# Performance work log

Hardware: AMD Instinct MI355X
Metric: run time of the kernel (lower is better)

## Reference

```python
import jax, jax.numpy as jnp
import numpy as np

N_NODES = 50000

def _gcn_layer(x, src, dst, W, b, n_nodes):
    # x: [N, F_in]; src/dst: [E+N] (self-loops already appended)
    h = x @ W  # [N, F_out]
    deg = jax.ops.segment_sum(jnp.ones_like(dst, dtype=h.dtype), dst, num_segments=n_nodes)
    dinv = jnp.where(deg > 0, jax.lax.rsqrt(deg), 0.0)  # deg^{-1/2}
    norm = dinv[src] * dinv[dst]  # [E+N]
    msg = h[src] * norm[:, None]  # gather + scale
    out = jax.ops.segment_sum(msg, dst, num_segments=n_nodes)  # scatter-add
    return out + b

def setup_inputs() -> dict:
    key = jax.random.key(0)
    k1, k2, k3, k4 = jax.random.split(key, 4)
    d = 128
    E = 800000
    x = jax.random.normal(k1, (N_NODES, d), dtype=jnp.float32)
    edge_index = jax.random.randint(k2, (2, E), 0, N_NODES, dtype=jnp.int64)
    W1 = jax.random.normal(k3, (d, d), dtype=jnp.float32) / np.sqrt(d)
    b1 = jnp.zeros((d,), dtype=jnp.float32)
    W2 = jax.random.normal(k4, (d, d), dtype=jnp.float32) / np.sqrt(d)
    b2 = jnp.zeros((d,), dtype=jnp.float32)
    return {"x": x, "edge_index": edge_index, "W1": W1, "b1": b1, "W2": W2, "b2": b2}

def reference(x, edge_index, W1, b1, W2, b2):
    n = x.shape[0]
    loops = jnp.arange(n, dtype=edge_index.dtype)
    src = jnp.concatenate([edge_index[0], loops])  # add self-loops
    dst = jnp.concatenate([edge_index[1], loops])
    h = _gcn_layer(x, src, dst, W1, b1, n)
    h = jax.nn.relu(h)
    z = _gcn_layer(h, src, dst, W2, b2, n)
    return z
```

## Files before the change

### kernel.cpp

```cpp
#include <hip/hip_runtime.h>
#include <hip/hip_fp16.h>

#define NF 128
#define DMAX 64

typedef _Float16 half8  __attribute__((ext_vector_type(8)));
typedef _Float16 half4v __attribute__((ext_vector_type(4)));
typedef float    floatx4 __attribute__((ext_vector_type(4)));

__global__ __launch_bounds__(256) void z_k(
    int* __restrict__ cnt, int N, int zb,
    const float* __restrict__ W1, const float* __restrict__ W2,
    __half* __restrict__ WT1, __half* __restrict__ WT2)
{
    int b = blockIdx.x;
    if (b < zb) {
        int i = b * 256 + threadIdx.x;
        if (i <= N) cnt[i] = 0;
        return;
    }
    int idx = (b - zb) * 256 + threadIdx.x;
    const float* W = (idx < 16384) ? W1 : W2;
    __half* WT     = (idx < 16384) ? WT1 : WT2;
    int j = idx & 16383;
    int nn = j & 127, k = j >> 7;
    WT[nn * NF + k] = __float2half(W[k * NF + nn]);
}

__device__ __forceinline__ void gemm1raw_body(
    const float* __restrict__ X, const __half* __restrict__ WT,
    float* __restrict__ H32, int M, int bid, __half (*wlds)[136])
{
    const int tid = threadIdx.x;
    {
        int r = tid >> 2;
        int c0 = (tid & 3) * 32;
        const half8* s = (const half8*)(WT + (size_t)r * NF + c0);
        half8* d = (half8*)&wlds[r][c0];
        #pragma unroll
        for (int j = 0; j < 4; j++) d[j] = s[j];
    }
    __syncthreads();

    const int wave = tid >> 6, lane = tid & 63;
    const int quad = lane >> 4, l15 = lane & 15;
    const int rowA = bid * 128 + wave * 16 + l15;
    const int rowc = (rowA < M) ? rowA : (M - 1);

    half8 afr[4];
    #pragma unroll
    for (int kc = 0; kc < 4; kc++) {
        const floatx4* p = (const floatx4*)(X + (size_t)rowc * NF + kc * 32 + quad * 8);
        floatx4 u = p[0], v = p[1];
        half8 a;
        a[0] = (_Float16)u[0]; a[1] = (_Float16)u[1];
        a[2] = (_Float16)u[2]; a[3] = (_Float16)u[3];
        a[4] = (_Float16)v[0]; a[5] = (_Float16)v[1];
        a[6] = (_Float16)v[2]; a[7] = (_Float16)v[3];
        afr[kc] = a;
    }

    floatx4 acc[8];
    #pragma unroll
    for (int ct = 0; ct < 8; ct++) { floatx4 z = {0.f, 0.f, 0.f, 0.f}; acc[ct] = z; }

    #pragma unroll
    for (int kc = 0; kc < 4; kc++) {
        #pragma unroll
        for (int ct = 0; ct < 8; ct++) {
            half8 b = *(const half8*)&wlds[ct * 16 + l15][kc * 32 + quad * 8];
            acc[ct] = __builtin_amdgcn_mfma_f32_16x16x32_f16(afr[kc], b, acc[ct], 0, 0, 0);
        }
    }

    const int orow0 = bid * 128 + wave * 16 + quad * 4;
    #pragma unroll
    for (int r = 0; r < 4; r++) {
        int orow = orow0 + r;
        if (orow < M) {
            #pragma unroll
            for (int ct = 0; ct < 8; ct++)
                H32[(size_t)orow * NF + ct * 16 + l15] = acc[ct][r];
        }
    }
}

__global__ __launch_bounds__(512) void mix_k(
    const int* __restrict__ src, const int* __restrict__ dst,
    int* __restrict__ cnt, int* __restrict__ csrF, int* __restrict__ ovf,
    int E, int N,
    const float* __restrict__ X, const __half* __restrict__ WT,
    float* __restrict__ H32, int GB)
{
    __shared__ __half wlds[128][136];
    const int b = blockIdx.x;
    const bool isGemm = ((b % 5) == 0) && (b / 5 < GB);
    if (isGemm) {
        gemm1raw_body(X, WT, H32, N, b / 5, wlds);
        return;
    }
    const int fid = (b < 5 * GB) ? (b - (b / 5 + 1)) : (b - GB);
    int e = fid * 512 + (int)threadIdx.x;
    if (e < E) {
        int d = dst[e], s = src[e];
        int pos = atomicAdd(&cnt[d], 1);
        if (pos < DMAX) {
            csrF[(size_t)d * DMAX + pos] = s;
        } else {
            int o = atomicAdd(&cnt[N], 1);
            ovf[2 * o] = d; ovf[2 * o + 1] = s;
        }
    }
}

__global__ __launch_bounds__(256) void scale_k(
    const float* __restrict__ H32, const int* __restrict__ cnt,
    __half* __restrict__ H16, int n)
{
    int i = blockIdx.x * 256 + threadIdx.x;
    int row = i >> 4, j = i & 15;
    if (row >= n) return;
    float dv = rsqrtf((float)cnt[row] + 1.0f);
    const floatx4* p = (const floatx4*)(H32 + (size_t)row * NF + j * 8);
    floatx4 u = p[0], v = p[1];
    half8 h;
    h[0] = (_Float16)(u[0] * dv); h[1] = (_Float16)(u[1] * dv);
    h[2] = (_Float16)(u[2] * dv); h[3] = (_Float16)(u[3] * dv);
    h[4] = (_Float16)(v[0] * dv); h[5] = (_Float16)(v[1] * dv);
    h[6] = (_Float16)(v[2] * dv); h[7] = (_Float16)(v[3] * dv);
    *(half8*)&H16[(size_t)row * NF + j * 8] = h;
}

__device__ __forceinline__ void gather2w(
    const half8* __restrict__ hs8, const int* __restrict__ csrF,
    const int* __restrict__ cnt, int nA, int n,
    int g, int fl, int lane, floatx4& ac0, floatx4& ac1,
    const int* __restrict__ ovf, int novf)
{
    const int ep  = g & 1;
    const int isB = g >> 1;
    const int nB  = nA + 1;

    int cntA = (nA < n) ? cnt[nA] : 0;
    int cntB = (nB < n) ? cnt[nB] : 0;
    const int ccA = min(cntA, DMAX), ccB = min(cntB, DMAX);

    int idxA = (lane < ccA) ? __builtin_nontemporal_load(&csrF[(size_t)nA * DMAX + lane]) : 0;
    int idxB = (lane < ccB) ? __builtin_nontemporal_load(&csrF[(size_t)nB * DMAX + lane]) : 0;

    if (ep == 0) {
        int nd = isB ? nB : nA;
        if (nd < n) {
            half8 s = hs8[(size_t)nd * 16 + fl];
            ac0[0] += (float)s[0]; ac0[1] += (float)s[1];
            ac0[2] += (float)s[2]; ac0[3] += (float)s[3];
            ac1[0] += (float)s[4]; ac1[1] += (float)s[5];
            ac1[2] += (float)s[6]; ac1[3] += (float)s[7];
        }
    }

    const int myc  = isB ? ccB : ccA;
    const int maxc = max(ccA, ccB);
    for (int j = 0; j < maxc; j += 16) {
        int s[8];
        half8 v[8];
        #pragma unroll
        for (int t = 0; t < 8; t++) {
            int e = j + 2 * t + ep;
            int eA = min(e, ccA - 1); eA = (eA < 0) ? 0 : eA;
            int eB = min(e, ccB - 1); eB = (eB < 0) ? 0 : eB;
            int sa = __shfl(idxA, eA, 64);
            int sb = __shfl(idxB, eB, 64);
            s[t] = isB ? sb : sa;
        }
        #pragma unroll
        for (int t = 0; t < 8; t++)
            v[t] = hs8[(size_t)s[t] * 16 + fl];
        #pragma unroll
        for (int t = 0; t < 8; t++) {
            if (j + 2 * t + ep < myc) {
                ac0[0] += (float)v[t][0]; ac0[1] += (float)v[t][1];
                ac0[2] += (float)v[t][2]; ac0[3] += (float)v[t][3];
                ac1[0] += (float)v[t][4]; ac1[1] += (float)v[t][5];
                ac1[2] += (float)v[t][6]; ac1[3] += (float)v[t][7];
            }
        }
    }

    if (novf > 0 && ep == 0) {
        int myN = isB ? nB : nA;
        for (int i = 0; i < novf; i++) {
            int d = ovf[2 * i];
            if (d == myN) {
                half8 v = hs8[(size_t)ovf[2 * i + 1] * 16 + fl];
                ac0[0] += (float)v[0]; ac0[1] += (float)v[1];
                ac0[2] += (float)v[2]; ac0[3] += (float)v[3];
                ac1[0] += (float)v[4]; ac1[1] += (float)v[5];
                ac1[2] += (float)v[6]; ac1[3] += (float)v[7];
            }
        }
    }

    #pragma unroll
    for (int q = 0; q < 4; q++) {
        ac0[q] += __shfl_xor(ac0[q], 16, 64);
        ac1[q] += __shfl_xor(ac1[q], 16, 64);
    }
}

__global__ __launch_bounds__(512) void aggmm_k(
    const __half* __restrict__ hs, const int* __restrict__ csrF,
    const int* __restrict__ cnt, const float* __restrict__ bias,
    const __half* __restrict__ WT, __half* __restrict__ Hout, int n,
    const int* __restrict__ ovf)
{
    __shared__ __half alds[16][136];
    const int tid = threadIdx.x;
    const int wave = tid >> 6, lane = tid & 63;
    const int g = lane >> 4, fl = lane & 15;
    const int nb0 = blockIdx.x * 16;
    const int nA = nb0 + wave * 2;
    const int novf = cnt[n];

    floatx4 ac0 = {0.f, 0.f, 0.f, 0.f}, ac1 = {0.f, 0.f, 0.f, 0.f};
    gather2w((const half8*)hs, csrF, cnt, nA, n, g, fl, lane, ac0, ac1, ovf, novf);

    if ((g & 1) == 0) {
        int node = nA + (g >> 1);
        int row  = wave * 2 + (g >> 1);
        half8 hv;
        if (node < n) {
            float dv = rsqrtf((float)cnt[node] + 1.0f);
            const floatx4 bv0 = *(const floatx4*)&bias[fl * 8];
            const floatx4 bv1 = *(const floatx4*)&bias[fl * 8 + 4];
            hv[0] = (_Float16)fmaxf(dv * ac0[0] + bv0[0], 0.f);
            hv[1] = (_Float16)fmaxf(dv * ac0[1] + bv0[1], 0.f);
            hv[2] = (_Float16)fmaxf(dv * ac0[2] + bv0[2], 0.f);
            hv[3] = (_Float16)fmaxf(dv * ac0[3] + bv0[3], 0.f);
            hv[4] = (_Float16)fmaxf(dv * ac1[0] + bv1[0], 0.f);
            hv[5] = (_Float16)fmaxf(dv * ac1[1] + bv1[1], 0.f);
            hv[6] = (_Float16)fmaxf(dv * ac1[2] + bv1[2], 0.f);
            hv[7] = (_Float16)fmaxf(dv * ac1[3] + bv1[3], 0.f);
        } else {
            #pragma unroll
            for (int i = 0; i < 8; i++) hv[i] = (_Float16)0.f;
        }
        *(half8*)&alds[row][fl * 8] = hv;
    }
    __syncthreads();

    const int quad = lane >> 4, l15 = lane & 15;
    const int ct = wave;
    half8 afr[4];
    #pragma unroll
    for (int kc = 0; kc < 4; kc++)
        afr[kc] = *(const half8*)&alds[l15][kc * 32 + quad * 8];

    floatx4 o0 = {0.f, 0.f, 0.f, 0.f};
    #pragma unroll
    for (int kc = 0; kc < 4; kc++) {
        half8 b = *(const half8*)(WT + (size_t)(ct * 16 + l15) * NF + kc * 32 + quad * 8);
        o0 = __builtin_amdgcn_mfma_f32_16x16x32_f16(afr[kc], b, o0, 0, 0, 0);
    }

    #pragma unroll
    for (int r = 0; r < 4; r++) {
        int node = nb0 + quad * 4 + r;
        if (node < n) {
            float dv = rsqrtf((float)cnt[node] + 1.0f);
            Hout[(size_t)node * NF + ct * 16 + l15] = __float2half(o0[r] * dv);
        }
    }
}

__global__ __launch_bounds__(256) void agg4_k(
    const __half* __restrict__ hs, const int* __restrict__ csrF,
    const int* __restrict__ cnt, const float* __restrict__ bias,
    float* __restrict__ outf, int n, const int* __restrict__ ovf)
{
    const int tid = threadIdx.x;
    const int wave = tid >> 6, lane = tid & 63;
    const int g = lane >> 4, fl = lane & 15;
    const int nA = blockIdx.x * 8 + wave * 2;
    if (nA >= n) return;
    const int novf = cnt[n];

    floatx4 ac0 = {0.f, 0.f, 0.f, 0.f}, ac1 = {0.f, 0.f, 0.f, 0.f};
    gather2w((const half8*)hs, csrF, cnt, nA, n, g, fl, lane, ac0, ac1, ovf, novf);

    if ((g & 1) == 0) {
        int node = nA + (g >> 1);
        if (node < n) {
            float dv = rsqrtf((float)cnt[node] + 1.0f);
            const floatx4 bv0 = *(const floatx4*)&bias[fl * 8];
            const floatx4 bv1 = *(const floatx4*)&bias[fl * 8 + 4];
            floatx4 w0, w1;
            w0[0] = dv * ac0[0] + bv0[0]; w0[1] = dv * ac0[1] + bv0[1];
            w0[2] = dv * ac0[2] + bv0[2]; w0[3] = dv * ac0[3] + bv0[3];
            w1[0] = dv * ac1[0] + bv1[0]; w1[1] = dv * ac1[1] + bv1[1];
            w1[2] = dv * ac1[2] + bv1[2]; w1[3] = dv * ac1[3] + bv1[3];
            *(floatx4*)(outf + (size_t)node * NF + fl * 8)     = w0;
            *(floatx4*)(outf + (size_t)node * NF + fl * 8 + 4) = w1;
        }
    }
}


extern "C" void kernel_launch(void* const* d_in, const int* in_sizes, int n_in,
                              void* d_out, int out_size, void* d_ws, size_t ws_size,
                              hipStream_t stream) {
    const float* x  = (const float*)d_in[0];
    const int*   ei = (const int*)d_in[1];
    const float* W1 = (const float*)d_in[2];
    const float* b1 = (const float*)d_in[3];
    const float* W2 = (const float*)d_in[4];
    const float* b2 = (const float*)d_in[5];
    float* out = (float*)d_out;

    const int N = in_sizes[0] / NF;
    const int E = in_sizes[1] / 2;
    const int* src = ei;
    const int* dst = ei + E;

    char* ws = (char*)d_ws;
    size_t off = 0;
    auto alloc = [&](size_t bytes) {
        void* p = ws + off;
        off += bytes;
        off = (off + 63) & ~(size_t)63;
        return p;
    };
    int*    cnt  = (int*)alloc((size_t)(N + 1) * 4);
    int*    csrF = (int*)alloc((size_t)N * DMAX * 4);
    int*    ovf  = (int*)alloc((size_t)E * 2 * 4);
    float*  H32  = (float*)alloc((size_t)N * NF * 4);
    __half* WT1  = (__half*)alloc((size_t)NF * NF * 2);
    __half* WT2  = (__half*)alloc((size_t)NF * NF * 2);
    __half* H16  = (__half*)alloc((size_t)N * NF * 2);
    __half* A16  = (__half*)alloc((size_t)N * NF * 2);

    int zb  = (N + 1 + 255) / 256;
    int GB  = (N + 127) / 128;
    int fb  = (E + 511) / 512;
    int sb  = (N * 16 + 255) / 256;
    int mb  = (N + 15) / 16;
    int ab  = (N + 7) / 8;

    z_k<<<zb + 128, 256, 0, stream>>>(cnt, N, zb, W1, W2, WT1, WT2);
    mix_k<<<fb + GB, 512, 0, stream>>>(src, dst, cnt, csrF, ovf, E, N,
                                       x, WT1, H32, GB);
    scale_k<<<sb, 256, 0, stream>>>(H32, cnt, H16, N);
    aggmm_k<<<mb, 512, 0, stream>>>(H16, csrF, cnt, b1, WT2, A16, N, ovf);
    agg4_k<<<ab, 256, 0, stream>>>(A16, csrF, cnt, b2, out, N, ovf);
}
```

Before: 209.7 us.

## Precompute degrees in a partitioned LDS histogram and fuse scaling into GEMM1

```diff
diff --git a/kernel.cpp b/kernel.cpp
--- a/kernel.cpp
+++ b/kernel.cpp
@@ -2,24 +2,55 @@
 #include <hip/hip_fp16.h>
 
 #define NF 128
+#define KC 64
+#define NPART 4
+#define NPMAX 12544
 #define DMAX 64
 
 typedef _Float16 half8  __attribute__((ext_vector_type(8)));
-typedef _Float16 half4v __attribute__((ext_vector_type(4)));
 typedef float    floatx4 __attribute__((ext_vector_type(4)));
 
-__global__ __launch_bounds__(256) void z_k(
-    int* __restrict__ cnt, int N, int zb,
+__global__ __launch_bounds__(512) void prep_k(
+    const int* __restrict__ dst, unsigned char* __restrict__ pcnt,
+    int* __restrict__ scnt, int E, int N, int Ec, int zb,
     const float* __restrict__ W1, const float* __restrict__ W2,
     __half* __restrict__ WT1, __half* __restrict__ WT2)
 {
-    int b = blockIdx.x;
-    if (b < zb) {
-        int i = b * 256 + threadIdx.x;
-        if (i <= N) cnt[i] = 0;
+    __shared__ int lcnt[NPMAX];
+    const int b = blockIdx.x;
+    const int CB = KC * NPART;
+    if (b < CB) {
+        const int p = b & 3, c = b >> 2;
+        const int Np = (N + 3) >> 2;
+        const int lo = p * Np, hi = min(lo + Np, N);
+        const int sz = hi - lo;
+        for (int i = threadIdx.x; i < sz; i += 512) lcnt[i] = 0;
+        __syncthreads();
+
+        const int e0 = c * Ec, e1 = min(e0 + Ec, E);
+        for (int e = e0 + (int)threadIdx.x * 4; e + 3 < e1; e += 512 * 4) {
+            int4 d = *(const int4*)(dst + e);
+            if (d.x >= lo && d.x < hi) atomicAdd(&lcnt[d.x - lo], 1);
+            if (d.y >= lo && d.y < hi) atomicAdd(&lcnt[d.y - lo], 1);
+            if (d.z >= lo && d.z < hi) atomicAdd(&lcnt[d.z - lo], 1);
+            if (d.w >= lo && d.w < hi) atomicAdd(&lcnt[d.w - lo], 1);
+        }
+        int rem0 = e0 + ((e1 - e0) & ~3);
+        for (int e = rem0 + (int)threadIdx.x; e < e1; e += 512) {
+            int d = dst[e];
+            if (d >= lo && d < hi) atomicAdd(&lcnt[d - lo], 1);
+        }
+        __syncthreads();
+        for (int i = threadIdx.x; i < sz; i += 512)
+            pcnt[(size_t)c * N + lo + i] = (unsigned char)lcnt[i];
         return;
     }
-    int idx = (b - zb) * 256 + threadIdx.x;
+    if (b < CB + zb) {
+        int i = (b - CB) * 512 + threadIdx.x;
+        if (i <= N) scnt[i] = 0;
+        return;
+    }
+    int idx = (b - CB - zb) * 512 + threadIdx.x;
     const float* W = (idx < 16384) ? W1 : W2;
     __half* WT     = (idx < 16384) ? WT1 : WT2;
     int j = idx & 16383;
@@ -27,9 +58,11 @@
     WT[nn * NF + k] = __float2half(W[k * NF + nn]);
 }
 
-__device__ __forceinline__ void gemm1raw_body(
+__device__ __forceinline__ void gemm1_body(
     const float* __restrict__ X, const __half* __restrict__ WT,
-    float* __restrict__ H32, int M, int bid, __half (*wlds)[136])
+    const unsigned char* __restrict__ pcnt, int* __restrict__ deg,
+    __half* __restrict__ H, int M, int bid,
+    __half (*wlds)[136], int* degl)
 {
     const int tid = threadIdx.x;
     {
@@ -39,6 +72,16 @@
         half8* d = (half8*)&wlds[r][c0];
         #pragma unroll
         for (int j = 0; j < 4; j++) d[j] = s[j];
+    }
+    if (tid < 128) {
+        int nd = bid * 128 + tid;
+        int dt = 0;
+        if (nd < M) {
+            #pragma unroll 8
+            for (int c = 0; c < KC; c++) dt += pcnt[(size_t)c * M + nd];
+            deg[nd] = dt;
+        }
+        degl[tid] = dt;
     }
     __syncthreads();
 
@@ -73,67 +116,52 @@
         }
     }
 
-    const int orow0 = bid * 128 + wave * 16 + quad * 4;
+    const int lrow0 = wave * 16 + quad * 4;
     #pragma unroll
     for (int r = 0; r < 4; r++) {
-        int orow = orow0 + r;
+        int orow = bid * 128 + lrow0 + r;
         if (orow < M) {
+            float dv = rsqrtf((float)degl[lrow0 + r] + 1.0f);
             #pragma unroll
             for (int ct = 0; ct < 8; ct++)
-                H32[(size_t)orow * NF + ct * 16 + l15] = acc[ct][r];
+                H[(size_t)orow * NF + ct * 16 + l15] = __float2half(acc[ct][r] * dv);
         }
     }
 }
 
 __global__ __launch_bounds__(512) void mix_k(
     const int* __restrict__ src, const int* __restrict__ dst,
-    int* __restrict__ cnt, int* __restrict__ csrF, int* __restrict__ ovf,
+    int* __restrict__ scnt, int* __restrict__ csrF, int* __restrict__ ovf,
     int E, int N,
     const float* __restrict__ X, const __half* __restrict__ WT,
-    float* __restrict__ H32, int GB)
+    const unsigned char* __restrict__ pcnt, int* __restrict__ deg,
+    __half* __restrict__ H16, int GB)
 {
     __shared__ __half wlds[128][136];
+    __shared__ int degl[128];
     const int b = blockIdx.x;
     const bool isGemm = ((b % 5) == 0) && (b / 5 < GB);
     if (isGemm) {
-        gemm1raw_body(X, WT, H32, N, b / 5, wlds);
+        gemm1_body(X, WT, pcnt, deg, H16, N, b / 5, wlds, degl);
         return;
     }
     const int fid = (b < 5 * GB) ? (b - (b / 5 + 1)) : (b - GB);
     int e = fid * 512 + (int)threadIdx.x;
     if (e < E) {
         int d = dst[e], s = src[e];
-        int pos = atomicAdd(&cnt[d], 1);
+        int pos = atomicAdd(&scnt[d], 1);
         if (pos < DMAX) {
-            csrF[(size_t)d * DMAX + pos] = s;
+            __builtin_nontemporal_store(s, &csrF[(size_t)d * DMAX + pos]);
         } else {
-            int o = atomicAdd(&cnt[N], 1);
+            int o = atomicAdd(&scnt[N], 1);
             ovf[2 * o] = d; ovf[2 * o + 1] = s;
         }
     }
-}
-
-__global__ __launch_bounds__(256) void scale_k(
-    const float* __restrict__ H32, const int* __restrict__ cnt,
-    __half* __restrict__ H16, int n)
-{
-    int i = blockIdx.x * 256 + threadIdx.x;
-    int row = i >> 4, j = i & 15;
-    if (row >= n) return;
-    float dv = rsqrtf((float)cnt[row] + 1.0f);
-    const floatx4* p = (const floatx4*)(H32 + (size_t)row * NF + j * 8);
-    floatx4 u = p[0], v = p[1];
-    half8 h;
-    h[0] = (_Float16)(u[0] * dv); h[1] = (_Float16)(u[1] * dv);
-    h[2] = (_Float16)(u[2] * dv); h[3] = (_Float16)(u[3] * dv);
-    h[4] = (_Float16)(v[0] * dv); h[5] = (_Float16)(v[1] * dv);
-    h[6] = (_Float16)(v[2] * dv); h[7] = (_Float16)(v[3] * dv);
-    *(half8*)&H16[(size_t)row * NF + j * 8] = h;
 }
 
 __device__ __forceinline__ void gather2w(
     const half8* __restrict__ hs8, const int* __restrict__ csrF,
-    const int* __restrict__ cnt, int nA, int n,
+    const int* __restrict__ deg, int nA, int n,
     int g, int fl, int lane, floatx4& ac0, floatx4& ac1,
     const int* __restrict__ ovf, int novf)
 {
@@ -141,8 +169,8 @@
     const int isB = g >> 1;
     const int nB  = nA + 1;
 
-    int cntA = (nA < n) ? cnt[nA] : 0;
-    int cntB = (nB < n) ? cnt[nB] : 0;
+    int cntA = (nA < n) ? deg[nA] : 0;
+    int cntB = (nB < n) ? deg[nB] : 0;
     const int ccA = min(cntA, DMAX), ccB = min(cntB, DMAX);
 
     int idxA = (lane < ccA) ? __builtin_nontemporal_load(&csrF[(size_t)nA * DMAX + lane]) : 0;
@@ -210,9 +238,9 @@
 
 __global__ __launch_bounds__(512) void aggmm_k(
     const __half* __restrict__ hs, const int* __restrict__ csrF,
-    const int* __restrict__ cnt, const float* __restrict__ bias,
-    const __half* __restrict__ WT, __half* __restrict__ Hout, int n,
-    const int* __restrict__ ovf)
+    const int* __restrict__ deg, const int* __restrict__ scnt,
+    const float* __restrict__ bias, const __half* __restrict__ WT,
+    __half* __restrict__ Hout, int n, const int* __restrict__ ovf)
 {
     __shared__ __half alds[16][136];
     const int tid = threadIdx.x;
@@ -220,17 +248,17 @@
     const int g = lane >> 4, fl = lane & 15;
     const int nb0 = blockIdx.x * 16;
     const int nA = nb0 + wave * 2;
-    const int novf = cnt[n];
+    const int novf = scnt[n];
 
     floatx4 ac0 = {0.f, 0.f, 0.f, 0.f}, ac1 = {0.f, 0.f, 0.f, 0.f};
-    gather2w((const half8*)hs, csrF, cnt, nA, n, g, fl, lane, ac0, ac1, ovf, novf);
+    gather2w((const half8*)hs, csrF, deg, nA, n, g, fl, lane, ac0, ac1, ovf, novf);
 
     if ((g & 1) == 0) {
         int node = nA + (g >> 1);
         int row  = wave * 2 + (g >> 1);
         half8 hv;
         if (node < n) {
-            float dv = rsqrtf((float)cnt[node] + 1.0f);
+            float dv = rsqrtf((float)deg[node] + 1.0f);
             const floatx4 bv0 = *(const floatx4*)&bias[fl * 8];
             const floatx4 bv1 = *(const floatx4*)&bias[fl * 8 + 4];
             hv[0] = (_Float16)fmaxf(dv * ac0[0] + bv0[0], 0.f);
@@ -267,7 +295,7 @@
     for (int r = 0; r < 4; r++) {
         int node = nb0 + quad * 4 + r;
         if (node < n) {
-            float dv = rsqrtf((float)cnt[node] + 1.0f);
+            float dv = rsqrtf((float)deg[node] + 1.0f);
             Hout[(size_t)node * NF + ct * 16 + l15] = __float2half(o0[r] * dv);
         }
     }
@@ -275,23 +303,24 @@
 
 __global__ __launch_bounds__(256) void agg4_k(
     const __half* __restrict__ hs, const int* __restrict__ csrF,
-    const int* __restrict__ cnt, const float* __restrict__ bias,
-    float* __restrict__ outf, int n, const int* __restrict__ ovf)
+    const int* __restrict__ deg, const int* __restrict__ scnt,
+    const float* __restrict__ bias, float* __restrict__ outf, int n,
+    const int* __restrict__ ovf)
 {
     const int tid = threadIdx.x;
     const int wave = tid >> 6, lane = tid & 63;
     const int g = lane >> 4, fl = lane & 15;
     const int nA = blockIdx.x * 8 + wave * 2;
     if (nA >= n) return;
-    const int novf = cnt[n];
+    const int novf = scnt[n];
 
     floatx4 ac0 = {0.f, 0.f, 0.f, 0.f}, ac1 = {0.f, 0.f, 0.f, 0.f};
-    gather2w((const half8*)hs, csrF, cnt, nA, n, g, fl, lane, ac0, ac1, ovf, novf);
+    gather2w((const half8*)hs, csrF, deg, nA, n, g, fl, lane, ac0, ac1, ovf, novf);
 
     if ((g & 1) == 0) {
         int node = nA + (g >> 1);
         if (node < n) {
-            float dv = rsqrtf((float)cnt[node] + 1.0f);
+            float dv = rsqrtf((float)deg[node] + 1.0f);
             const floatx4 bv0 = *(const floatx4*)&bias[fl * 8];
             const floatx4 bv1 = *(const floatx4*)&bias[fl * 8 + 4];
             floatx4 w0, w1;
@@ -330,26 +359,28 @@
         off = (off + 63) & ~(size_t)63;
         return p;
     };
-    int*    cnt  = (int*)alloc((size_t)(N + 1) * 4);
+    unsigned char* pcnt = (unsigned char*)alloc((size_t)KC * N);
+    int*    scnt = (int*)alloc((size_t)(N + 1) * 4);
+    int*    deg  = (int*)alloc((size_t)N * 4);
     int*    csrF = (int*)alloc((size_t)N * DMAX * 4);
     int*    ovf  = (int*)alloc((size_t)E * 2 * 4);
-    float*  H32  = (float*)alloc((size_t)N * NF * 4);
     __half* WT1  = (__half*)alloc((size_t)NF * NF * 2);
     __half* WT2  = (__half*)alloc((size_t)NF * NF * 2);
     __half* H16  = (__half*)alloc((size_t)N * NF * 2);
     __half* A16  = (__half*)alloc((size_t)N * NF * 2);
 
-    int zb  = (N + 1 + 255) / 256;
+    int Ec  = (((E + KC - 1) / KC) + 3) & ~3;
+    int zb  = (N + 1 + 511) / 512;
+    int tb  = 64;
     int GB  = (N + 127) / 128;
     int fb  = (E + 511) / 512;
-    int sb  = (N * 16 + 255) / 256;
     int mb  = (N + 15) / 16;
     int ab  = (N + 7) / 8;
 
-    z_k<<<zb + 128, 256, 0, stream>>>(cnt, N, zb, W1, W2, WT1, WT2);
-    mix_k<<<fb + GB, 512, 0, stream>>>(src, dst, cnt, csrF, ovf, E, N,
-                                       x, WT1, H32, GB);
-    scale_k<<<sb, 256, 0, stream>>>(H32, cnt, H16, N);
-    aggmm_k<<<mb, 512, 0, stream>>>(H16, csrF, cnt, b1, WT2, A16, N, ovf);
-    agg4_k<<<ab, 256, 0, stream>>>(A16, csrF, cnt, b2, out, N, ovf);
-}
+    prep_k<<<KC * NPART + zb + tb, 512, 0, stream>>>(
+        dst, pcnt, scnt, E, N, Ec, zb, W1, W2, WT1, WT2);
+    mix_k<<<GB + fb, 512, 0, stream>>>(src, dst, scnt, csrF, ovf, E, N,
+                                       x, WT1, pcnt, deg, H16, GB);
+    aggmm_k<<<mb, 512, 0, stream>>>(H16, csrF, deg, scnt, b1, WT2, A16, N, ovf);
+    agg4_k<<<ab, 256, 0, stream>>>(A16, csrF, deg, scnt, b2, out, N, ovf);
+}
```

Result: slower. 223.7 us (+6.7%).
